# Kernel tuning notes

Measured on AMD Instinct MI355X. Metric: run time of the kernel, lower is better.

Reference implementation:

```python
import math
import jax, jax.numpy as jnp
import numpy as np

D_MODEL = 896
N_HEADS = 14
D_HEAD = D_MODEL // N_HEADS  # 64
ROPE_BASE = 10000.0
LN_EPS = 1e-5
B, N = 8, 1024


def setup_inputs() -> dict:
    key = jax.random.key(0)
    ks = jax.random.split(key, 12)
    s = 1.0 / math.sqrt(D_MODEL)
    return {
        "node_features": jax.random.normal(ks[0], (B, N, D_MODEL), jnp.float32),
        "adj": jax.random.uniform(ks[1], (N, N), jnp.float32),
        "wind_dirs": jax.random.uniform(ks[2], (B, N), jnp.float32),
        "bearings": jax.random.uniform(ks[3], (N, N), jnp.float32),
        "Wq": jax.random.normal(ks[4], (D_MODEL, D_MODEL), jnp.float32) * s,
        "Wk": jax.random.normal(ks[5], (D_MODEL, D_MODEL), jnp.float32) * s,
        "Wv": jax.random.normal(ks[6], (D_MODEL, D_MODEL), jnp.float32) * s,
        "Wo": jax.random.normal(ks[7], (D_MODEL, D_MODEL), jnp.float32) * s,
        "ln_g": jnp.ones((D_MODEL,), jnp.float32),
        "ln_b": jnp.zeros((D_MODEL,), jnp.float32),
        "wind_w": jax.random.normal(ks[8], (2, N_HEADS), jnp.float32) * (1.0 / math.sqrt(2.0)),
        "wind_b": jnp.zeros((N_HEADS,), jnp.float32),
    }


def _layernorm(x, g, b):
    mu = jnp.mean(x, axis=-1, keepdims=True)
    var = jnp.var(x, axis=-1, keepdims=True)
    return (x - mu) * jax.lax.rsqrt(var + LN_EPS) * g + b


def _apply_rotary(x, cos_h, sin_h):
    # x: (B,H,N,d_head); cos_h/sin_h: (N, d_head//2)
    d_half = x.shape[-1] // 2
    x1, x2 = x[..., :d_half], x[..., d_half:]
    return jnp.concatenate([x1 * cos_h - x2 * sin_h, x2 * cos_h + x1 * sin_h], axis=-1)


def reference(node_features, adj, wind_dirs, bearings, Wq, Wk, Wv, Wo, ln_g, ln_b, wind_w, wind_b):
    Bb, Nn, D = node_features.shape
    residual = node_features
    x = _layernorm(node_features, ln_g, ln_b)

    def proj(W):
        return (x @ W).reshape(Bb, Nn, N_HEADS, D_HEAD).transpose(0, 2, 1, 3)  # (B,H,N,dh)

    Q, K, V = proj(Wq), proj(Wk), proj(Wv)

    # RoPE: cos/sin halves (first d_half entries of the duplicated freq table)
    inv_freq = 1.0 / (ROPE_BASE ** (jnp.arange(0, D_HEAD, 2, dtype=jnp.float32) / D_HEAD))
    freqs = jnp.arange(Nn, dtype=jnp.float32)[:, None] * inv_freq[None, :]  # (N, dh/2)
    cos_h, sin_h = jnp.cos(freqs), jnp.sin(freqs)
    Q = _apply_rotary(Q, cos_h, sin_h)
    K = _apply_rotary(K, cos_h, sin_h)

    attn = jnp.einsum("bhqd,bhkd->bhqk", Q, K) / math.sqrt(D_HEAD)
    adj_mask = (adj > 0)[None, None, :, :]
    attn = jnp.where(adj_mask, attn, -1e30)

    # wind-direction dynamic edge bias
    reverse_bearings = (bearings.T + 180.0) % 360.0  # (N,N)
    alignment = jnp.cos(jnp.deg2rad(wind_dirs[:, :, None] - reverse_bearings[None]))  # (B,N,N)
    dist_feat = jnp.broadcast_to(adj[None], (Bb, Nn, Nn))
    edge_features = jnp.stack([alignment, dist_feat], axis=-1)  # (B,N,N,2)
    wind_bias = jnp.tanh(edge_features @ wind_w + wind_b)  # (B,N,N,H)
    attn = attn + wind_bias.transpose(0, 3, 1, 2)  # (B,H,N,N)

    attn = jax.nn.softmax(attn, axis=-1)  # dropout is identity in eval
    out = jnp.einsum("bhqk,bhkd->bhqd", attn, V)
    out = out.transpose(0, 2, 1, 3).reshape(Bb, Nn, D) @ Wo
    return residual + out
```

## Files before the change

### kernel.cpp

```cpp
#include <hip/hip_runtime.h>
#include <hip/hip_bf16.h>
#include <math.h>

#define B_ 8
#define N_ 1024
#define H_ 14
#define DH_ 64
#define D_ 896
#define M_ (B_*N_)
#define DQKV_ 2688

typedef __attribute__((ext_vector_type(8))) short bf16x8;
typedef __attribute__((ext_vector_type(4))) short bf16x4;
typedef __attribute__((ext_vector_type(4))) float f32x4;
typedef __attribute__((ext_vector_type(4))) unsigned u32x4;

__device__ __forceinline__ float bf2f(short s){
  unsigned u = ((unsigned)(unsigned short)s) << 16;
  union { unsigned u; float f; } c; c.u = u; return c.f;
}
__device__ __forceinline__ short f2bf(float f){
  union { float f; unsigned u; } c; c.f = f;
  unsigned u = c.u;
  unsigned r = (u + 0x7FFFu + ((u >> 16) & 1u)) >> 16;
  return (short)(unsigned short)r;
}
__device__ __forceinline__ float asf(unsigned u){
  union { unsigned u; float f; } c; c.u = u; return c.f;
}

__global__ __launch_bounds__(256) void ln_kernel(const float* __restrict__ x,
                                                 const float* __restrict__ g,
                                                 const float* __restrict__ bb,
                                                 short* __restrict__ y)
{
  int row = blockIdx.x;
  const float* xr = x + (size_t)row * D_;
  float s = 0.f, s2 = 0.f;
  for (int i = threadIdx.x; i < D_; i += 256){
    float v = xr[i]; s += v; s2 = fmaf(v, v, s2);
  }
  #pragma unroll
  for (int off = 32; off > 0; off >>= 1){
    s  += __shfl_down(s,  off, 64);
    s2 += __shfl_down(s2, off, 64);
  }
  __shared__ float rs_[4], rs2_[4];
  int wv = threadIdx.x >> 6;
  if ((threadIdx.x & 63) == 0){ rs_[wv] = s; rs2_[wv] = s2; }
  __syncthreads();
  float ts  = rs_[0] + rs_[1] + rs_[2] + rs_[3];
  float ts2 = rs2_[0] + rs2_[1] + rs2_[2] + rs2_[3];
  float mu  = ts * (1.f / D_);
  float var = ts2 * (1.f / D_) - mu * mu;
  float rstd = rsqrtf(var + 1e-5f);
  short* yr = y + (size_t)row * D_;
  for (int i = threadIdx.x; i < D_; i += 256){
    yr[i] = f2bf((xr[i] - mu) * rstd * g[i] + bb[i]);
  }
}

__global__ __launch_bounds__(256) void transpose_kernel(
    const float* __restrict__ Wq, const float* __restrict__ Wk,
    const float* __restrict__ Wv, const float* __restrict__ Wo,
    short* __restrict__ WqkvT, short* __restrict__ WoT)
{
  __shared__ short t[64][72];
  int z = blockIdx.z;
  const float* W = (z == 0) ? Wq : (z == 1) ? Wk : (z == 2) ? Wv : Wo;
  int kb = blockIdx.x * 64, nb = blockIdx.y * 64;
  int c0 = (threadIdx.x & 7) * 8;
  int r0 = threadIdx.x >> 3;
  #pragma unroll
  for (int rr = 0; rr < 64; rr += 32){
    const float* src = &W[(size_t)(kb + r0 + rr) * D_ + nb + c0];
    float4 a = *(const float4*)src;
    float4 b = *(const float4*)(src + 4);
    short* dstl = &t[r0 + rr][c0];
    dstl[0] = f2bf(a.x); dstl[1] = f2bf(a.y); dstl[2] = f2bf(a.z); dstl[3] = f2bf(a.w);
    dstl[4] = f2bf(b.x); dstl[5] = f2bf(b.y); dstl[6] = f2bf(b.z); dstl[7] = f2bf(b.w);
  }
  __syncthreads();
  short* dst = (z < 3) ? (WqkvT + (size_t)(z * D_) * D_) : WoT;
  #pragma unroll
  for (int rr = 0; rr < 64; rr += 32){
    int n = nb + r0 + rr;
    bf16x8 v;
    #pragma unroll
    for (int j = 0; j < 8; j++) v[j] = t[c0 + j][r0 + rr];
    *(bf16x8*)&dst[(size_t)n * D_ + kb + c0] = v;
  }
}

__global__ __launch_bounds__(256) void prep_kernel(
    const float* __restrict__ adj, const float* __restrict__ brg,
    unsigned* __restrict__ csb, short* __restrict__ adjT)
{
  int kt = blockIdx.x, qt = blockIdx.y;
  int r  = threadIdx.x >> 2;
  int c0 = (threadIdx.x & 3) * 16;
  {
    int k = kt * 64 + r;
    const float* bp = brg + (size_t)k * N_ + qt * 64 + c0;
    unsigned* cp = csb + (size_t)k * N_ + qt * 64 + c0;
    #pragma unroll
    for (int i = 0; i < 16; i += 4){
      float4 bv = *(const float4*)(bp + i);
      float b4[4] = { bv.x, bv.y, bv.z, bv.w };
      unsigned o[4];
      #pragma unroll
      for (int j = 0; j < 4; j++){
        float Br = (b4[j] + 180.f) * 0.017453292519943295f;
        float sB, cB;
        __sincosf(Br, &sB, &cB);
        o[j] = ((unsigned)(unsigned short)f2bf(cB)) |
               (((unsigned)(unsigned short)f2bf(sB)) << 16);
      }
      *(uint4*)(cp + i) = make_uint4(o[0], o[1], o[2], o[3]);
    }
  }
  __shared__ short tt[64][72];
  {
    int q = qt * 64 + r;
    const float* ap = adj + (size_t)q * N_ + kt * 64 + c0;
    #pragma unroll
    for (int i = 0; i < 16; i += 4){
      float4 av = *(const float4*)(ap + i);
      tt[r][c0 + i]     = f2bf(av.x);
      tt[r][c0 + i + 1] = f2bf(av.y);
      tt[r][c0 + i + 2] = f2bf(av.z);
      tt[r][c0 + i + 3] = f2bf(av.w);
    }
  }
  __syncthreads();
  {
    int k = kt * 64 + r;
    short* op = adjT + (size_t)k * N_ + qt * 64 + c0;
    bf16x8 v0, v1;
    #pragma unroll
    for (int j = 0; j < 8; j++){ v0[j] = tt[c0 + j][r]; v1[j] = tt[c0 + 8 + j][r]; }
    *(bf16x8*)op = v0;
    *(bf16x8*)(op + 8) = v1;
  }
}

__global__ __launch_bounds__(256) void gemm_bt(const short* __restrict__ A,
                                               const short* __restrict__ Bt,
                                               short* __restrict__ C,
                                               float* __restrict__ Cf,
                                               const float* __restrict__ residf,
                                               int N)
{
  const int K = D_;
  __shared__ short As[128 * 32];
  __shared__ short Bs[128 * 32];
  int tid  = threadIdx.x;
  int wave = tid >> 6;
  int lane = tid & 63;
  int quad = lane >> 4;
  int l16  = lane & 15;
  int wr = wave >> 1, wc = wave & 1;
  int m0 = blockIdx.x * 128;
  int n0 = blockIdx.y * 128;

  f32x4 acc[4][4];
  #pragma unroll
  for (int i = 0; i < 4; i++)
    #pragma unroll
    for (int j = 0; j < 4; j++)
      acc[i][j] = (f32x4){0.f, 0.f, 0.f, 0.f};

  for (int k0 = 0; k0 < K; k0 += 32){
    __syncthreads();
    #pragma unroll
    for (int it = 0; it < 2; ++it){
      int c   = tid + it * 256;
      int row = c >> 2;
      int cc  = c & 3;
      const short* ga = A  + (size_t)(m0 + row) * K + k0 + cc * 8;
      const short* gb = Bt + (size_t)(n0 + row) * K + k0 + cc * 8;
      short* la = As + (size_t)(wave * 64 + it * 256) * 8;
      short* lb = Bs + (size_t)(wave * 64 + it * 256) * 8;
      __builtin_amdgcn_global_load_lds((const __attribute__((address_space(1))) void*)ga,
                                       (__attribute__((address_space(3))) void*)la, 16, 0, 0);
      __builtin_amdgcn_global_load_lds((const __attribute__((address_space(1))) void*)gb,
                                       (__attribute__((address_space(3))) void*)lb, 16, 0, 0);
    }
    __syncthreads();

    bf16x8 af[4], bfr[4];
    #pragma unroll
    for (int i = 0; i < 4; i++)
      af[i] = *(const bf16x8*)(As + (size_t)(wr * 64 + i * 16 + l16) * 32 + quad * 8);
    #pragma unroll
    for (int j = 0; j < 4; j++)
      bfr[j] = *(const bf16x8*)(Bs + (size_t)(wc * 64 + j * 16 + l16) * 32 + quad * 8);
    #pragma unroll
    for (int i = 0; i < 4; i++)
      #pragma unroll
      for (int j = 0; j < 4; j++)
        acc[i][j] = __builtin_amdgcn_mfma_f32_16x16x32_bf16(af[i], bfr[j], acc[i][j], 0, 0, 0);
  }

  #pragma unroll
  for (int i = 0; i < 4; i++){
    #pragma unroll
    for (int rr = 0; rr < 4; rr++){
      int r = m0 + wr * 64 + i * 16 + quad * 4 + rr;
      size_t rowoff = (size_t)r * N;
      #pragma unroll
      for (int j = 0; j < 4; j++){
        int cidx = n0 + wc * 64 + j * 16 + l16;
        float v = acc[i][j][rr];
        if (Cf){
          Cf[rowoff + cidx] = v + residf[rowoff + cidx];
        } else {
          C[rowoff + cidx] = f2bf(v);
        }
      }
    }
  }
}

__global__ __launch_bounds__(256) void rope_kernel(short* __restrict__ QKV)
{
  int idx  = blockIdx.x * 256 + threadIdx.x;
  int mrow = idx / D_;
  int r    = idx - mrow * D_;
  int mat  = r / 448;
  int hi   = r - mat * 448;
  int h    = hi >> 5;
  int i    = hi & 31;
  int n    = mrow & (N_ - 1);
  float invf = exp2f(-(float)i * 0.4152410118609203f);
  float ang  = (float)n * invf;
  float sv, cv;
  __sincosf(ang, &sv, &cv);
  size_t base = (size_t)mrow * DQKV_ + (size_t)mat * D_ + h * DH_ + i;
  float x1 = bf2f(QKV[base]);
  float x2 = bf2f(QKV[base + 32]);
  float o1 = x1 * cv - x2 * sv;
  float o2 = x2 * cv + x1 * sv;
  if (mat == 0){ o1 *= 0.125f; o2 *= 0.125f; }
  QKV[base]      = f2bf(o1);
  QKV[base + 32] = f2bf(o2);
}

#define M0_ 12.0f
__global__ __launch_bounds__(512, 4) void attn_kernel(
    const short* __restrict__ QKV,
    const unsigned* __restrict__ csb,
    const short* __restrict__ adjT,
    const float* __restrict__ wind_dirs,
    const float* __restrict__ wind_w,
    const float* __restrict__ wind_b,
    short* __restrict__ outb)
{
  __shared__ short K_s[64 * 72];
  __shared__ short V_t[64 * 76];
  __shared__ short P_s[128 * 76];

  int bid = blockIdx.x;
  int qt  = bid & 7;
  int hh  = (bid >> 3) % H_;
  int b   = bid / (8 * H_);
  int q0  = qt * 128;

  int t    = threadIdx.x;
  int w    = t >> 6;
  int lane = t & 63;
  int quad = lane >> 4;
  int l16  = lane & 15;

  const short* qp = QKV + ((size_t)(b * N_) + q0 + w * 16 + l16) * DQKV_ + hh * DH_;
  bf16x8 qf0 = *(const bf16x8*)(qp + quad * 8);
  bf16x8 qf1 = *(const bf16x8*)(qp + 32 + quad * 8);

  float cA[4], sA[4];
  #pragma unroll
  for (int rr = 0; rr < 4; rr++){
    float wd = wind_dirs[(size_t)b * N_ + q0 + w * 16 + quad * 4 + rr];
    float A  = wd * 0.017453292519943295f;
    sA[rr] = __sinf(A);
    cA[rr] = __cosf(A);
  }
  float w0 = wind_w[hh];
  float w1 = wind_w[H_ + hh];
  float wb = wind_b[hh];

  float l[4] = {0.f, 0.f, 0.f, 0.f};
  f32x4 O[4];
  #pragma unroll
  for (int dc = 0; dc < 4; dc++) O[dc] = (f32x4){0.f, 0.f, 0.f, 0.f};

  int kr  = t >> 3, kc8 = (t & 7) * 8;
  int vk2 = (t >> 4) * 2, vd4 = (t & 15) * 4;

  for (int kt = 0; kt < 16; ++kt){
    int k0 = kt * 64;
    __syncthreads();
    {
      const short* kg = QKV + ((size_t)(b * N_) + k0 + kr) * DQKV_ + D_ + hh * DH_ + kc8;
      *(bf16x8*)(K_s + kr * 72 + kc8) = *(const bf16x8*)kg;
      const short* vg = QKV + ((size_t)(b * N_) + k0 + vk2) * DQKV_ + 2 * D_ + hh * DH_ + vd4;
      bf16x4 v0 = *(const bf16x4*)vg;
      bf16x4 v1 = *(const bf16x4*)(vg + DQKV_);
      #pragma unroll
      for (int j = 0; j < 4; j++){
        unsigned pv = ((unsigned)(unsigned short)v0[j]) |
                      (((unsigned)(unsigned short)v1[j]) << 16);
        *(unsigned*)(V_t + (vd4 + j) * 76 + vk2) = pv;
      }
    }
    __syncthreads();

    u32x4 cs4a[4]; bf16x4 av4a[4];
    #pragma unroll
    for (int jc = 0; jc < 4; jc++){
      size_t off = (size_t)(k0 + jc * 16 + l16) * N_ + q0 + w * 16 + quad * 4;
      cs4a[jc] = *(const u32x4*)(csb + off);
      av4a[jc] = *(const bf16x4*)(adjT + off);
    }

    f32x4 S[4];
    #pragma unroll
    for (int jc = 0; jc < 4; jc++){
      S[jc] = (f32x4){0.f, 0.f, 0.f, 0.f};
      bf16x8 kf0 = *(const bf16x8*)(K_s + (jc * 16 + l16) * 72 + quad * 8);
      bf16x8 kf1 = *(const bf16x8*)(K_s + (jc * 16 + l16) * 72 + 32 + quad * 8);
      S[jc] = __builtin_amdgcn_mfma_f32_16x16x32_bf16(qf0, kf0, S[jc], 0, 0, 0);
      S[jc] = __builtin_amdgcn_mfma_f32_16x16x32_bf16(qf1, kf1, S[jc], 0, 0, 0);
    }

    #pragma unroll
    for (int jc = 0; jc < 4; jc++){
      #pragma unroll
      for (int rr = 0; rr < 4; rr++){
        unsigned u = cs4a[jc][rr];
        float cB = asf(u << 16);
        float sB = asf(u & 0xffff0000u);
        float av = bf2f(av4a[jc][rr]);
        float align = cA[rr] * cB + sA[rr] * sB;
        float z  = fmaf(align, w0, fmaf(av, w1, wb));
        float e2 = __expf(2.f * z);
        float bias = 1.f - 2.f * __builtin_amdgcn_rcpf(e2 + 1.f);
        float sv = (av > 0.f ? S[jc][rr] : -1e30f) + (bias - M0_);
        float e = __expf(sv);
        S[jc][rr] = e;
        l[rr] += e;
        P_s[(w * 16 + quad * 4 + rr) * 76 + jc * 16 + l16] = f2bf(e);
      }
    }

    #pragma unroll
    for (int kc = 0; kc < 2; kc++){
      const short* pp = P_s + (w * 16 + l16) * 76 + kc * 32 + quad * 8;
      bf16x4 p0 = *(const bf16x4*)pp;
      bf16x4 p1 = *(const bf16x4*)(pp + 4);
      bf16x8 pf = { p0[0], p0[1], p0[2], p0[3], p1[0], p1[1], p1[2], p1[3] };
      #pragma unroll
      for (int dc = 0; dc < 4; dc++){
        const short* vp = V_t + (dc * 16 + l16) * 76 + kc * 32 + quad * 8;
        bf16x4 u0 = *(const bf16x4*)vp;
        bf16x4 u1 = *(const bf16x4*)(vp + 4);
        bf16x8 vf = { u0[0], u0[1], u0[2], u0[3], u1[0], u1[1], u1[2], u1[3] };
        O[dc] = __builtin_amdgcn_mfma_f32_16x16x32_bf16(pf, vf, O[dc], 0, 0, 0);
      }
    }
  }

  float rl[4];
  #pragma unroll
  for (int rr = 0; rr < 4; rr++){
    float rs = l[rr];
    rs += __shfl_xor(rs, 1);
    rs += __shfl_xor(rs, 2);
    rs += __shfl_xor(rs, 4);
    rs += __shfl_xor(rs, 8);
    rl[rr] = 1.f / rs;
  }
  short* op = outb + ((size_t)(b * N_) + q0 + w * 16) * D_ + hh * DH_;
  #pragma unroll
  for (int rr = 0; rr < 4; rr++)
    #pragma unroll
    for (int dc = 0; dc < 4; dc++)
      op[(size_t)(quad * 4 + rr) * D_ + dc * 16 + l16] = f2bf(O[dc][rr] * rl[rr]);
}

extern "C" void kernel_launch(void* const* d_in, const int* in_sizes, int n_in,
                              void* d_out, int out_size, void* d_ws, size_t ws_size,
                              hipStream_t stream)
{
  const float* nf   = (const float*)d_in[0];
  const float* adj  = (const float*)d_in[1];
  const float* wdir = (const float*)d_in[2];
  const float* brg  = (const float*)d_in[3];
  const float* Wq   = (const float*)d_in[4];
  const float* Wk   = (const float*)d_in[5];
  const float* Wv   = (const float*)d_in[6];
  const float* Wo   = (const float*)d_in[7];
  const float* lng  = (const float*)d_in[8];
  const float* lnb  = (const float*)d_in[9];
  const float* ww   = (const float*)d_in[10];
  const float* wbb  = (const float*)d_in[11];
  float* out = (float*)d_out;

  short* xln   = (short*)d_ws;
  short* WqkvT = xln   + (size_t)M_ * D_;
  short* WoT   = WqkvT + (size_t)DQKV_ * D_;
  short* QKV   = WoT   + (size_t)D_ * D_;
  unsigned* csb = (unsigned*)(QKV + (size_t)M_ * DQKV_);
  short* adjT  = (short*)(csb + (size_t)N_ * N_);

  ln_kernel<<<M_, 256, 0, stream>>>(nf, lng, lnb, xln);
  transpose_kernel<<<dim3(14, 14, 4), 256, 0, stream>>>(Wq, Wk, Wv, Wo, WqkvT, WoT);
  prep_kernel<<<dim3(16, 16), 256, 0, stream>>>(adj, brg, csb, adjT);
  gemm_bt<<<dim3(M_ / 128, DQKV_ / 128), 256, 0, stream>>>(xln, WqkvT, QKV, nullptr, nullptr, DQKV_);
  rope_kernel<<<(M_ * D_) / 256, 256, 0, stream>>>(QKV);
  attn_kernel<<<B_ * H_ * 8, 512, 0, stream>>>(QKV, csb, adjT, wdir, ww, wbb, xln);
  gemm_bt<<<dim3(M_ / 128, D_ / 128), 256, 0, stream>>>(xln, WoT, nullptr, out, nf, D_);
}
```

Before: 378.6 us.

## Fuse RoPE into QKV GEMM, precompute wind alignment, prefetch K/V, use exp2

Moves RoPE into the QKV GEMM epilogue so the separate RoPE pass over QKV is dropped, and folds the softmax scale and log2e into the Q scale. When workspace allows, adds a kernel that precomputes per-batch alignment cosines so the attention inner loop loads one bf16 instead of doing the trig combine. The attention loop now register-prefetches the next K/V tile, switches to exp2 with pre-multiplied constants, and raises wave priority around the MFMA blocks. The new alignT buffer adds a B*N*N bf16 read stream to attention, and the RoPE pairing in the epilogue depends on the accumulator column mapping matching head layout.

```diff
diff --git a/kernel.cpp b/kernel.cpp
--- a/kernel.cpp
+++ b/kernel.cpp
@@ -9,6 +9,10 @@
 #define D_ 896
 #define M_ (B_*N_)
 #define DQKV_ 2688
+
+#define TWO_LOG2E_ 2.8853900817779268f
+#define BIAS_C_   (-15.869645449778597f)
+#define QSCALE_     0.18033688011112043f
 
 typedef __attribute__((ext_vector_type(8))) short bf16x8;
 typedef __attribute__((ext_vector_type(4))) short bf16x4;
@@ -144,12 +148,49 @@
   }
 }
 
+__global__ __launch_bounds__(256) void align_kernel(const float* __restrict__ brg,
+                                                    const float* __restrict__ wdir,
+                                                    short* __restrict__ alignT)
+{
+  int kt = blockIdx.x;
+  int b  = blockIdx.y;
+  __shared__ float cA[N_], sA[N_];
+  for (int q = threadIdx.x; q < N_; q += 256){
+    float A = wdir[(size_t)b * N_ + q] * 0.017453292519943295f;
+    float s, c; __sincosf(A, &s, &c);
+    sA[q] = s; cA[q] = c;
+  }
+  __syncthreads();
+  int q4 = threadIdx.x * 4;
+  for (int kr = 0; kr < 64; kr++){
+    int k = kt * 64 + kr;
+    float4 bv = *(const float4*)(brg + (size_t)k * N_ + q4);
+    float b4[4] = { bv.x, bv.y, bv.z, bv.w };
+    unsigned oo[2];
+    #pragma unroll
+    for (int p = 0; p < 2; p++){
+      unsigned lo = 0, hi = 0;
+      #pragma unroll
+      for (int j = 0; j < 2; j++){
+        int qq = q4 + p * 2 + j;
+        float Br = (b4[p * 2 + j] + 180.f) * 0.017453292519943295f;
+        float sB, cB; __sincosf(Br, &sB, &cB);
+        float al = fmaf(cA[qq], cB, sA[qq] * sB);
+        unsigned v = (unsigned)(unsigned short)f2bf(al);
+        if (j == 0) lo = v; else hi = v;
+      }
+      oo[p] = lo | (hi << 16);
+    }
+    *(uint2*)(alignT + ((size_t)b * N_ + k) * N_ + q4) = make_uint2(oo[0], oo[1]);
+  }
+}
+
 __global__ __launch_bounds__(256) void gemm_bt(const short* __restrict__ A,
                                                const short* __restrict__ Bt,
                                                short* __restrict__ C,
                                                float* __restrict__ Cf,
                                                const float* __restrict__ residf,
-                                               int N)
+                                               int N, int rope)
 {
   const int K = D_;
   __shared__ short As[128 * 32];
@@ -202,6 +243,33 @@
         acc[i][j] = __builtin_amdgcn_mfma_f32_16x16x32_bf16(af[i], bfr[j], acc[i][j], 0, 0, 0);
   }
 
+  if (rope){
+    int cb  = n0 + wc * 64;
+    int mat = cb / D_;
+    if (mat < 2){
+      float scale = (mat == 0) ? QSCALE_ : 1.0f;
+      float invf0 = exp2f(-0.4152410118609203f * (float)l16);
+      float invf1 = invf0 * 0.01f;
+      #pragma unroll
+      for (int i = 0; i < 4; i++){
+        #pragma unroll
+        for (int rr = 0; rr < 4; rr++){
+          int r = m0 + wr * 64 + i * 16 + quad * 4 + rr;
+          float nseq = (float)(r & (N_ - 1));
+          float s0, c0v, s1, c1v;
+          __sincosf(nseq * invf0, &s0, &c0v);
+          __sincosf(nseq * invf1, &s1, &c1v);
+          float x1 = acc[i][0][rr], x2 = acc[i][2][rr];
+          acc[i][0][rr] = (x1 * c0v - x2 * s0) * scale;
+          acc[i][2][rr] = (x2 * c0v + x1 * s0) * scale;
+          x1 = acc[i][1][rr]; x2 = acc[i][3][rr];
+          acc[i][1][rr] = (x1 * c1v - x2 * s1) * scale;
+          acc[i][3][rr] = (x2 * c1v + x1 * s1) * scale;
+        }
+      }
+    }
+  }
+
   #pragma unroll
   for (int i = 0; i < 4; i++){
     #pragma unroll
@@ -222,35 +290,15 @@
   }
 }
 
-__global__ __launch_bounds__(256) void rope_kernel(short* __restrict__ QKV)
-{
-  int idx  = blockIdx.x * 256 + threadIdx.x;
-  int mrow = idx / D_;
-  int r    = idx - mrow * D_;
-  int mat  = r / 448;
-  int hi   = r - mat * 448;
-  int h    = hi >> 5;
-  int i    = hi & 31;
-  int n    = mrow & (N_ - 1);
-  float invf = exp2f(-(float)i * 0.4152410118609203f);
-  float ang  = (float)n * invf;
-  float sv, cv;
-  __sincosf(ang, &sv, &cv);
-  size_t base = (size_t)mrow * DQKV_ + (size_t)mat * D_ + h * DH_ + i;
-  float x1 = bf2f(QKV[base]);
-  float x2 = bf2f(QKV[base + 32]);
-  float o1 = x1 * cv - x2 * sv;
-  float o2 = x2 * cv + x1 * sv;
-  if (mat == 0){ o1 *= 0.125f; o2 *= 0.125f; }
-  QKV[base]      = f2bf(o1);
-  QKV[base + 32] = f2bf(o2);
-}
-
-#define M0_ 12.0f
+__global__ __launch_bounds__(512, 4)
+__global__ void attn_dummy();
+
+template<int PRE>
 __global__ __launch_bounds__(512, 4) void attn_kernel(
     const short* __restrict__ QKV,
     const unsigned* __restrict__ csb,
     const short* __restrict__ adjT,
+    const short* __restrict__ alignT,
     const float* __restrict__ wind_dirs,
     const float* __restrict__ wind_w,
     const float* __restrict__ wind_b,
@@ -277,16 +325,18 @@
   bf16x8 qf1 = *(const bf16x8*)(qp + 32 + quad * 8);
 
   float cA[4], sA[4];
-  #pragma unroll
-  for (int rr = 0; rr < 4; rr++){
-    float wd = wind_dirs[(size_t)b * N_ + q0 + w * 16 + quad * 4 + rr];
-    float A  = wd * 0.017453292519943295f;
-    sA[rr] = __sinf(A);
-    cA[rr] = __cosf(A);
-  }
-  float w0 = wind_w[hh];
-  float w1 = wind_w[H_ + hh];
-  float wb = wind_b[hh];
+  if (!PRE){
+    #pragma unroll
+    for (int rr = 0; rr < 4; rr++){
+      float wd = wind_dirs[(size_t)b * N_ + q0 + w * 16 + quad * 4 + rr];
+      float A  = wd * 0.017453292519943295f;
+      sA[rr] = __sinf(A);
+      cA[rr] = __cosf(A);
+    }
+  }
+  float w0m = wind_w[hh]      * TWO_LOG2E_;
+  float w1m = wind_w[H_ + hh] * TWO_LOG2E_;
+  float wbm = wind_b[hh]      * TWO_LOG2E_;
 
   float l[4] = {0.f, 0.f, 0.f, 0.f};
   f32x4 O[4];
@@ -295,34 +345,43 @@
 
   int kr  = t >> 3, kc8 = (t & 7) * 8;
   int vk2 = (t >> 4) * 2, vd4 = (t & 15) * 4;
+  const short* kg0 = QKV + ((size_t)(b * N_) + kr)  * DQKV_ + D_     + hh * DH_ + kc8;
+  const short* vg0 = QKV + ((size_t)(b * N_) + vk2) * DQKV_ + 2 * D_ + hh * DH_ + vd4;
+
+  bf16x8 pk  = *(const bf16x8*)kg0;
+  bf16x4 pv0 = *(const bf16x4*)vg0;
+  bf16x4 pv1 = *(const bf16x4*)(vg0 + DQKV_);
 
   for (int kt = 0; kt < 16; ++kt){
     int k0 = kt * 64;
     __syncthreads();
+    *(bf16x8*)(K_s + kr * 72 + kc8) = pk;
+    #pragma unroll
+    for (int j = 0; j < 4; j++){
+      unsigned pv = ((unsigned)(unsigned short)pv0[j]) |
+                    (((unsigned)(unsigned short)pv1[j]) << 16);
+      *(unsigned*)(V_t + (vd4 + j) * 76 + vk2) = pv;
+    }
+    __syncthreads();
+
     {
-      const short* kg = QKV + ((size_t)(b * N_) + k0 + kr) * DQKV_ + D_ + hh * DH_ + kc8;
-      *(bf16x8*)(K_s + kr * 72 + kc8) = *(const bf16x8*)kg;
-      const short* vg = QKV + ((size_t)(b * N_) + k0 + vk2) * DQKV_ + 2 * D_ + hh * DH_ + vd4;
-      bf16x4 v0 = *(const bf16x4*)vg;
-      bf16x4 v1 = *(const bf16x4*)(vg + DQKV_);
-      #pragma unroll
-      for (int j = 0; j < 4; j++){
-        unsigned pv = ((unsigned)(unsigned short)v0[j]) |
-                      (((unsigned)(unsigned short)v1[j]) << 16);
-        *(unsigned*)(V_t + (vd4 + j) * 76 + vk2) = pv;
-      }
-    }
-    __syncthreads();
-
-    u32x4 cs4a[4]; bf16x4 av4a[4];
+      int kn = (kt < 15) ? (k0 + 64) : k0;
+      pk  = *(const bf16x8*)(kg0 + (size_t)kn * DQKV_);
+      pv0 = *(const bf16x4*)(vg0 + (size_t)kn * DQKV_);
+      pv1 = *(const bf16x4*)(vg0 + (size_t)(kn + 1) * DQKV_);
+    }
+
+    u32x4 cs4a[4]; bf16x4 al4a[4]; bf16x4 av4a[4];
     #pragma unroll
     for (int jc = 0; jc < 4; jc++){
       size_t off = (size_t)(k0 + jc * 16 + l16) * N_ + q0 + w * 16 + quad * 4;
-      cs4a[jc] = *(const u32x4*)(csb + off);
+      if (PRE) al4a[jc] = *(const bf16x4*)(alignT + (size_t)b * N_ * N_ + off);
+      else     cs4a[jc] = *(const u32x4*)(csb + off);
       av4a[jc] = *(const bf16x4*)(adjT + off);
     }
 
     f32x4 S[4];
+    __builtin_amdgcn_s_setprio(1);
     #pragma unroll
     for (int jc = 0; jc < 4; jc++){
       S[jc] = (f32x4){0.f, 0.f, 0.f, 0.f};
@@ -331,27 +390,34 @@
       S[jc] = __builtin_amdgcn_mfma_f32_16x16x32_bf16(qf0, kf0, S[jc], 0, 0, 0);
       S[jc] = __builtin_amdgcn_mfma_f32_16x16x32_bf16(qf1, kf1, S[jc], 0, 0, 0);
     }
+    __builtin_amdgcn_s_setprio(0);
 
     #pragma unroll
     for (int jc = 0; jc < 4; jc++){
       #pragma unroll
       for (int rr = 0; rr < 4; rr++){
-        unsigned u = cs4a[jc][rr];
-        float cB = asf(u << 16);
-        float sB = asf(u & 0xffff0000u);
         float av = bf2f(av4a[jc][rr]);
-        float align = cA[rr] * cB + sA[rr] * sB;
-        float z  = fmaf(align, w0, fmaf(av, w1, wb));
-        float e2 = __expf(2.f * z);
-        float bias = 1.f - 2.f * __builtin_amdgcn_rcpf(e2 + 1.f);
-        float sv = (av > 0.f ? S[jc][rr] : -1e30f) + (bias - M0_);
-        float e = __expf(sv);
-        S[jc][rr] = e;
+        float align;
+        if (PRE){
+          align = bf2f(al4a[jc][rr]);
+        } else {
+          unsigned u = cs4a[jc][rr];
+          float cB = asf(u << 16);
+          float sB = asf(u & 0xffff0000u);
+          align = cA[rr] * cB + sA[rr] * sB;
+        }
+        float z2 = fmaf(align, w0m, fmaf(av, w1m, wbm));
+        float e2 = __builtin_amdgcn_exp2f(z2);
+        float rc = __builtin_amdgcn_rcpf(e2 + 1.f);
+        float bias2 = fmaf(-TWO_LOG2E_, rc, BIAS_C_);
+        float sv = (av > 0.f ? S[jc][rr] : -1e30f) + bias2;
+        float e = __builtin_amdgcn_exp2f(sv);
         l[rr] += e;
         P_s[(w * 16 + quad * 4 + rr) * 76 + jc * 16 + l16] = f2bf(e);
       }
     }
 
+    __builtin_amdgcn_s_setprio(1);
     #pragma unroll
     for (int kc = 0; kc < 2; kc++){
       const short* pp = P_s + (w * 16 + l16) * 76 + kc * 32 + quad * 8;
@@ -367,6 +433,7 @@
         O[dc] = __builtin_amdgcn_mfma_f32_16x16x32_bf16(pf, vf, O[dc], 0, 0, 0);
       }
     }
+    __builtin_amdgcn_s_setprio(0);
   }
 
   float rl[4];
@@ -405,18 +472,27 @@
   const float* wbb  = (const float*)d_in[11];
   float* out = (float*)d_out;
 
-  short* xln   = (short*)d_ws;
-  short* WqkvT = xln   + (size_t)M_ * D_;
-  short* WoT   = WqkvT + (size_t)DQKV_ * D_;
-  short* QKV   = WoT   + (size_t)D_ * D_;
-  unsigned* csb = (unsigned*)(QKV + (size_t)M_ * DQKV_);
-  short* adjT  = (short*)(csb + (size_t)N_ * N_);
+  short* base = (short*)d_ws;
+  size_t sh = 0;
+  short* xln   = base + sh;  sh += (size_t)M_ * D_;
+  short* WqkvT = base + sh;  sh += (size_t)DQKV_ * D_;
+  short* WoT   = base + sh;  sh += (size_t)D_ * D_;
+  short* QKV   = base + sh;  sh += (size_t)M_ * DQKV_;
+  unsigned* csb = (unsigned*)(base + sh); sh += (size_t)N_ * N_ * 2;
+  short* adjT  = base + sh;  sh += (size_t)N_ * N_;
+  short* alignT = base + sh; sh += (size_t)B_ * N_ * N_;
+  size_t need_pre = sh * sizeof(short);
+  bool pre = (ws_size >= need_pre);
 
   ln_kernel<<<M_, 256, 0, stream>>>(nf, lng, lnb, xln);
   transpose_kernel<<<dim3(14, 14, 4), 256, 0, stream>>>(Wq, Wk, Wv, Wo, WqkvT, WoT);
   prep_kernel<<<dim3(16, 16), 256, 0, stream>>>(adj, brg, csb, adjT);
-  gemm_bt<<<dim3(M_ / 128, DQKV_ / 128), 256, 0, stream>>>(xln, WqkvT, QKV, nullptr, nullptr, DQKV_);
-  rope_kernel<<<(M_ * D_) / 256, 256, 0, stream>>>(QKV);
-  attn_kernel<<<B_ * H_ * 8, 512, 0, stream>>>(QKV, csb, adjT, wdir, ww, wbb, xln);
-  gemm_bt<<<dim3(M_ / 128, D_ / 128), 256, 0, stream>>>(xln, WoT, nullptr, out, nf, D_);
-}
+  if (pre)
+    align_kernel<<<dim3(16, 8), 256, 0, stream>>>(brg, wdir, alignT);
+  gemm_bt<<<dim3(M_ / 128, DQKV_ / 128), 256, 0, stream>>>(xln, WqkvT, QKV, nullptr, nullptr, DQKV_, 1);
+  if (pre)
+    attn_kernel<1><<<B_ * H_ * 8, 512, 0, stream>>>(QKV, csb, adjT, alignT, wdir, ww, wbb, xln);
+  else
+    attn_kernel<0><<<B_ * H_ * 8, 512, 0, stream>>>(QKV, csb, adjT, alignT, wdir, ww, wbb, xln);
+  gemm_bt<<<dim3(M_ / 128, D_ / 128), 256, 0, stream>>>(xln, WoT, nullptr, out, nf, D_, 0);
+}
```

After: 405.7 us. 7.2% more time.
